# Performance work log

Measured on AMD Instinct MI355X. Metric: run time of the kernel, lower is better.

## Reference

```python
import jax, jax.numpy as jnp
import numpy as np

B, T, C, E, K = 4, 4096, 2048, 64, 8


def setup_inputs() -> dict:
    key = jax.random.key(0)
    k1, k2, k3 = jax.random.split(key, 3)
    hidden_states = jax.random.normal(k1, (B, T, C), dtype=jnp.float32)
    mask = jax.random.randint(k2, (B, T), 0, 2).astype(bool)
    gate_weight = jax.random.normal(k3, (E, C), dtype=jnp.float32) * 0.02
    gate_bias = jnp.zeros((E,), dtype=jnp.float32)
    expert_biases = jnp.zeros((E,), dtype=jnp.float32)
    return {
        "hidden_states": hidden_states,
        "mask": mask,
        "gate_weight": gate_weight,
        "gate_bias": gate_bias,
        "expert_biases": expert_biases,
    }


def reference(hidden_states, mask, gate_weight, gate_bias, expert_biases):
    Bc, Tc, Cc = hidden_states.shape
    n_experts = gate_weight.shape[0]
    x = hidden_states.reshape(-1, Cc)                 # [N, C]
    m = mask.reshape(-1)                              # [N]
    gate_output = x @ gate_weight.T + gate_bias       # [N, E]
    gate_probs = jax.nn.sigmoid(gate_output)
    gate_logits = gate_output + expert_biases
    _, top_k_indices = jax.lax.top_k(gate_logits, K)  # [N, K]
    top_k_probs = jnp.take_along_axis(gate_probs, top_k_indices, axis=-1)
    top_k_probs = top_k_probs / jnp.sum(top_k_probs, axis=-1, keepdims=True)
    # masked bincount of routed experts (only tokens where mask is True)
    weights = jnp.broadcast_to(m[:, None], top_k_indices.shape).astype(jnp.float32)
    expert_counts = jnp.zeros((n_experts,), jnp.float32).at[top_k_indices.reshape(-1)].add(weights.reshape(-1))
    avg_count = expert_counts.mean()
    maxvio = (expert_counts.max() - avg_count) / (avg_count + 1e-5)
    # note: the in-place expert_biases sign-update is a training-time, no-grad
    # side effect and does not change the returned values of this call.
    return top_k_indices, top_k_probs, maxvio
```

## Files before the change

### kernel.cpp

```cpp
#include <hip/hip_runtime.h>
#include <math.h>

#define NTOK   16384
#define CDIM   2048
#define NEXP   64
#define TOPK   8
#define GBLK   1024
#define NWAVE  8

typedef _Float16 f16x8 __attribute__((ext_vector_type(8)));
typedef float    f32x4 __attribute__((ext_vector_type(4)));

__global__ __launch_bounds__(256) void pack_w16_kernel(
    const float* __restrict__ W,
    _Float16* __restrict__ Wh, _Float16* __restrict__ Wl)
{
    int t    = blockIdx.x * 256 + threadIdx.x;
    int lane = t & 63;
    int nt   = (t >> 6) & 3;
    int s    = t >> 8;
    int e    = nt * 16 + (lane & 15);
    int k    = s * 32 + (lane >> 4) * 8;
    const float* src = W + (size_t)e * CDIM + k;
    #pragma unroll
    for (int j = 0; j < 8; j++) {
        float x = src[j];
        _Float16 h = (_Float16)x;
        Wh[(size_t)t * 8 + j] = h;
        Wl[(size_t)t * 8 + j] = (_Float16)(x - (float)h);
    }
}

__device__ __forceinline__ void mfma_step(
    const float4 v0, const float4 v1,
    const f16x8* __restrict__ bh, const f16x8* __restrict__ bl,
    f32x4* __restrict__ acc)
{
    float xr[8] = {v0.x, v0.y, v0.z, v0.w, v1.x, v1.y, v1.z, v1.w};
    f16x8 ah, al;
    #pragma unroll
    for (int j = 0; j < 8; j++) {
        _Float16 h = (_Float16)xr[j];
        ah[j] = h;
        al[j] = (_Float16)(xr[j] - (float)h);
    }
    #pragma unroll
    for (int nt = 0; nt < 4; nt++) {
        acc[nt] = __builtin_amdgcn_mfma_f32_16x16x32_f16(ah, bh[nt], acc[nt], 0, 0, 0);
        acc[nt] = __builtin_amdgcn_mfma_f32_16x16x32_f16(al, bh[nt], acc[nt], 0, 0, 0);
        acc[nt] = __builtin_amdgcn_mfma_f32_16x16x32_f16(ah, bl[nt], acc[nt], 0, 0, 0);
    }
}

__global__ __launch_bounds__(512, 8) void gate_fused_kernel(
    const float* __restrict__ x,
    const _Float16* __restrict__ Wh,
    const _Float16* __restrict__ Wl,
    const int*   __restrict__ mask,
    const float* __restrict__ gbias,
    const float* __restrict__ ebias,
    float*       __restrict__ out,
    float*       __restrict__ blockcnt)
{
    __shared__ f32x4 sacc[NWAVE][4][64];
    __shared__ unsigned int cnt[NEXP];
    const int tid  = threadIdx.x;
    const int lane = tid & 63;
    const int wid  = tid >> 6;
    if (tid < NEXP) cnt[tid] = 0u;

    const int tok0 = blockIdx.x * 16;
    const int col  = lane & 15;
    const int q    = lane >> 4;
    const float* xp = x + (size_t)(tok0 + col) * CDIM + wid * 256 + q * 8;
    const f16x8* bhp = (const f16x8*)Wh + (size_t)wid * 8 * 256 + lane;
    const f16x8* blp = (const f16x8*)Wl + (size_t)wid * 8 * 256 + lane;

    f32x4 acc[4];
    #pragma unroll
    for (int nt = 0; nt < 4; nt++) acc[nt] = (f32x4){0.f, 0.f, 0.f, 0.f};

    #pragma unroll 2
    for (int s = 0; s < 8; s++) {
        float4 v0 = *(const float4*)(xp + s * 32);
        float4 v1 = *(const float4*)(xp + s * 32 + 4);
        f16x8 bh[4], bl[4];
        #pragma unroll
        for (int nt = 0; nt < 4; nt++) {
            bh[nt] = bhp[s * 256 + nt * 64];
            bl[nt] = blp[s * 256 + nt * 64];
        }
        mfma_step(v0, v1, bh, bl, acc);
    }

    #pragma unroll
    for (int nt = 0; nt < 4; nt++) sacc[wid][nt][lane] = acc[nt];
    __syncthreads();

    if (wid == 0) {
        f32x4 zv[4];
        #pragma unroll
        for (int nt = 0; nt < 4; nt++) {
            f32x4 s = sacc[0][nt][lane];
            #pragma unroll
            for (int w = 1; w < NWAVE; w++) s += sacc[w][nt][lane];
            zv[nt] = s;
        }

        float gb[4], eb[4];
        #pragma unroll
        for (int nt = 0; nt < 4; nt++) {
            gb[nt] = gbias[nt * 16 + col];
            eb[nt] = ebias[nt * 16 + col];
        }

        #pragma unroll
        for (int r = 0; r < 4; r++) {
            const int t = tok0 + q * 4 + r;
            float z[4], sel[4];
            #pragma unroll
            for (int nt = 0; nt < 4; nt++) {
                z[nt]   = zv[nt][r] + gb[nt];
                sel[nt] = z[nt] + eb[nt];
            }

            int idxs[TOPK]; float probs[TOPK]; float psum = 0.f;
            #pragma unroll
            for (int rr = 0; rr < TOPK; rr++) {
                float bv = -INFINITY, bz = 0.f; int bidx = 1 << 30;
                #pragma unroll
                for (int nt = 0; nt < 4; nt++)
                    if (sel[nt] > bv) { bv = sel[nt]; bz = z[nt]; bidx = nt * 16 + col; }
                #pragma unroll
                for (int m = 1; m < 16; m <<= 1) {
                    float ov = __shfl_xor(bv, m);
                    float oz = __shfl_xor(bz, m);
                    int   oi = __shfl_xor(bidx, m);
                    if (ov > bv || (ov == bv && oi < bidx)) { bv = ov; bz = oz; bidx = oi; }
                }
                idxs[rr] = bidx;
                float p = 1.f / (1.f + expf(-bz));
                probs[rr] = p; psum += p;
                if ((bidx & 15) == col) sel[bidx >> 4] = -INFINITY;
            }
            float inv = 1.f / psum;
            if (col < TOPK) {
                out[(size_t)t * TOPK + col] = (float)idxs[col];
                out[(size_t)NTOK * TOPK + (size_t)t * TOPK + col] = probs[col] * inv;
                if (mask[t] != 0) atomicAdd(&cnt[idxs[col]], 1u);
            }
        }
        blockcnt[(size_t)blockIdx.x * NEXP + lane] = (float)cnt[lane];
    }
}

__global__ __launch_bounds__(256) void finalize_kernel(
    const float* __restrict__ blockcnt, float* __restrict__ out)
{
    __shared__ float ps[4][NEXP];
    const int t = threadIdx.x;
    const int e = t & 63, c = t >> 6;
    float s = 0.f;
    #pragma unroll 8
    for (int b = 0; b < GBLK / 4; b++)
        s += blockcnt[(size_t)(c * (GBLK / 4) + b) * NEXP + e];
    ps[c][e] = s;
    __syncthreads();
    if (t < 64) {
        float tot = ps[0][t] + ps[1][t] + ps[2][t] + ps[3][t];
        float mx = tot, sm = tot;
        #pragma unroll
        for (int o = 32; o > 0; o >>= 1) {
            mx = fmaxf(mx, __shfl_down(mx, o));
            sm += __shfl_down(sm, o);
        }
        if (t == 0) {
            float avg = sm / (float)NEXP;
            out[2 * NTOK * TOPK] = (mx - avg) / (avg + 1e-5f);
        }
    }
}

__global__ __launch_bounds__(256) void fused_fallback_kernel(
    const float* __restrict__ x, const int* __restrict__ mask,
    const float* __restrict__ W, const float* __restrict__ gbias,
    const float* __restrict__ ebias, float* __restrict__ out,
    unsigned int* __restrict__ counts)
{
    __shared__ float As[64][36];
    __shared__ float Bs[64][36];
    __shared__ float Lg[64][NEXP + 1];
    __shared__ float s_gb[NEXP], s_eb[NEXP];
    __shared__ unsigned int s_cnt[NEXP];
    const int tid = threadIdx.x;
    const int tx = tid & 15, ty = tid >> 4;
    const int m0 = blockIdx.x * 64;
    if (tid < NEXP) { s_gb[tid] = gbias[tid]; s_eb[tid] = ebias[tid]; s_cnt[tid] = 0u; }
    float acc[4][4] = {};
    for (int kb = 0; kb < CDIM; kb += 32) {
        __syncthreads();
        #pragma unroll
        for (int p = 0; p < 2; p++) {
            int lin = tid + p * 256; int m = lin >> 3; int c4 = (lin & 7) << 2;
            *(float4*)&As[m][c4] = *(const float4*)&x[(size_t)(m0 + m) * CDIM + kb + c4];
            *(float4*)&Bs[m][c4] = *(const float4*)&W[(size_t)m * CDIM + kb + c4];
        }
        __syncthreads();
        #pragma unroll
        for (int k4 = 0; k4 < 32; k4 += 4) {
            float4 a[4], b[4];
            #pragma unroll
            for (int i = 0; i < 4; i++) a[i] = *(const float4*)&As[ty * 4 + i][k4];
            #pragma unroll
            for (int j = 0; j < 4; j++) b[j] = *(const float4*)&Bs[tx * 4 + j][k4];
            #pragma unroll
            for (int i = 0; i < 4; i++)
                #pragma unroll
                for (int j = 0; j < 4; j++)
                    acc[i][j] += a[i].x * b[j].x + a[i].y * b[j].y
                               + a[i].z * b[j].z + a[i].w * b[j].w;
        }
    }
    __syncthreads();
    #pragma unroll
    for (int i = 0; i < 4; i++)
        #pragma unroll
        for (int j = 0; j < 4; j++)
            Lg[ty * 4 + i][tx * 4 + j] = acc[i][j] + s_gb[tx * 4 + j];
    __syncthreads();
    if (tid < 64) {
        const int g = m0 + tid;
        unsigned long long used = 0ull;
        int idxs[TOPK]; float probs[TOPK]; float psum = 0.f;
        #pragma unroll
        for (int k = 0; k < TOPK; k++) {
            float best = -INFINITY; int bi = 0;
            for (int n = 0; n < NEXP; n++) {
                if ((used >> n) & 1ull) continue;
                float vv = Lg[tid][n] + s_eb[n];
                if (vv > best) { best = vv; bi = n; }
            }
            used |= (1ull << bi);
            idxs[k] = bi;
            float p = 1.f / (1.f + expf(-Lg[tid][bi]));
            probs[k] = p; psum += p;
        }
        float inv = 1.f / psum;
        #pragma unroll
        for (int k = 0; k < TOPK; k++) {
            out[(size_t)g * TOPK + k] = (float)idxs[k];
            out[(size_t)NTOK * TOPK + (size_t)g * TOPK + k] = probs[k] * inv;
        }
        if (mask[g] != 0)
            #pragma unroll
            for (int k = 0; k < TOPK; k++) atomicAdd(&s_cnt[idxs[k]], 1u);
    }
    __syncthreads();
    if (tid < NEXP && s_cnt[tid] != 0u) atomicAdd(&counts[tid], s_cnt[tid]);
}

__global__ void finalize_atomic_kernel(const unsigned int* __restrict__ counts,
                                       float* __restrict__ out)
{
    const int t = threadIdx.x;
    float c  = (float)counts[t];
    float mx = c, sm = c;
    #pragma unroll
    for (int o = 32; o > 0; o >>= 1) {
        mx = fmaxf(mx, __shfl_down(mx, o));
        sm += __shfl_down(sm, o);
    }
    if (t == 0) {
        float avg = sm / (float)NEXP;
        out[2 * NTOK * TOPK] = (mx - avg) / (avg + 1e-5f);
    }
}

extern "C" void kernel_launch(void* const* d_in, const int* in_sizes, int n_in,
                              void* d_out, int out_size, void* d_ws, size_t ws_size,
                              hipStream_t stream)
{
    const float* x     = (const float*)d_in[0];
    const int*   mask  = (const int*)  d_in[1];
    const float* W     = (const float*)d_in[2];
    const float* gbias = (const float*)d_in[3];
    const float* ebias = (const float*)d_in[4];
    float* out = (float*)d_out;

    const size_t whB  = (size_t)NEXP * CDIM * sizeof(_Float16);
    const size_t bcB  = (size_t)GBLK * NEXP * sizeof(float);
    const size_t need = 2 * whB + bcB;

    if (ws_size >= need) {
        _Float16* Wh = (_Float16*)d_ws;
        _Float16* Wl = (_Float16*)((char*)d_ws + whB);
        float* blockcnt = (float*)((char*)d_ws + 2 * whB);

        pack_w16_kernel<<<64, 256, 0, stream>>>(W, Wh, Wl);
        gate_fused_kernel<<<GBLK, 512, 0, stream>>>(x, Wh, Wl, mask, gbias, ebias, out, blockcnt);
        finalize_kernel<<<1, 256, 0, stream>>>(blockcnt, out);
        return;
    }

    unsigned int* counts = (unsigned int*)d_ws;
    hipMemsetAsync(d_ws, 0, NEXP * sizeof(unsigned int), stream);
    fused_fallback_kernel<<<NTOK / 64, 256, 0, stream>>>(x, mask, W, gbias, ebias, out, counts);
    finalize_atomic_kernel<<<1, 64, 0, stream>>>(counts, out);
}
```

Before: 270.0 us.

## Process 32 tokens per block to reuse gate weight fragments across two tiles

Each block now computes two 16-token tiles, so every loaded split-f16 weight fragment feeds both tiles' MFMA chains. This halves the grid size and the weight reads per token. Top-k selection for the two tiles runs on two waves instead of one, and the per-block count write moves after an extra barrier. The cost is more registers (occupancy hint lowered from 8 to 4 waves) and a doubled shared accumulator buffer.

```diff
diff --git a/kernel.cpp b/kernel.cpp
--- a/kernel.cpp
+++ b/kernel.cpp
@@ -5,8 +5,9 @@
 #define CDIM   2048
 #define NEXP   64
 #define TOPK   8
-#define GBLK   1024
+#define TOKB   32
 #define NWAVE  8
+#define GBLK   (NTOK / TOKB)
 
 typedef _Float16 f16x8 __attribute__((ext_vector_type(8)));
 typedef float    f32x4 __attribute__((ext_vector_type(4)));
@@ -31,28 +32,19 @@
     }
 }
 
-__device__ __forceinline__ void mfma_step(
-    const float4 v0, const float4 v1,
-    const f16x8* __restrict__ bh, const f16x8* __restrict__ bl,
-    f32x4* __restrict__ acc)
+__device__ __forceinline__ void split_f16(
+    const float4 v0, const float4 v1, f16x8& ah, f16x8& al)
 {
     float xr[8] = {v0.x, v0.y, v0.z, v0.w, v1.x, v1.y, v1.z, v1.w};
-    f16x8 ah, al;
     #pragma unroll
     for (int j = 0; j < 8; j++) {
         _Float16 h = (_Float16)xr[j];
         ah[j] = h;
         al[j] = (_Float16)(xr[j] - (float)h);
     }
-    #pragma unroll
-    for (int nt = 0; nt < 4; nt++) {
-        acc[nt] = __builtin_amdgcn_mfma_f32_16x16x32_f16(ah, bh[nt], acc[nt], 0, 0, 0);
-        acc[nt] = __builtin_amdgcn_mfma_f32_16x16x32_f16(al, bh[nt], acc[nt], 0, 0, 0);
-        acc[nt] = __builtin_amdgcn_mfma_f32_16x16x32_f16(ah, bl[nt], acc[nt], 0, 0, 0);
-    }
-}
-
-__global__ __launch_bounds__(512, 8) void gate_fused_kernel(
+}
+
+__global__ __launch_bounds__(512, 4) void gate_fused_kernel(
     const float* __restrict__ x,
     const _Float16* __restrict__ Wh,
     const _Float16* __restrict__ Wl,
@@ -62,48 +54,69 @@
     float*       __restrict__ out,
     float*       __restrict__ blockcnt)
 {
-    __shared__ f32x4 sacc[NWAVE][4][64];
+    __shared__ f32x4 sacc[NWAVE][2][4][64];
     __shared__ unsigned int cnt[NEXP];
     const int tid  = threadIdx.x;
     const int lane = tid & 63;
     const int wid  = tid >> 6;
     if (tid < NEXP) cnt[tid] = 0u;
 
-    const int tok0 = blockIdx.x * 16;
+    const int tok0 = blockIdx.x * TOKB;
     const int col  = lane & 15;
     const int q    = lane >> 4;
-    const float* xp = x + (size_t)(tok0 + col) * CDIM + wid * 256 + q * 8;
+    const float* xpA = x + (size_t)(tok0 + col) * CDIM + wid * 256 + q * 8;
+    const float* xpB = xpA + (size_t)16 * CDIM;
     const f16x8* bhp = (const f16x8*)Wh + (size_t)wid * 8 * 256 + lane;
     const f16x8* blp = (const f16x8*)Wl + (size_t)wid * 8 * 256 + lane;
 
-    f32x4 acc[4];
-    #pragma unroll
-    for (int nt = 0; nt < 4; nt++) acc[nt] = (f32x4){0.f, 0.f, 0.f, 0.f};
+    f32x4 accA[4], accB[4];
+    #pragma unroll
+    for (int nt = 0; nt < 4; nt++) {
+        accA[nt] = (f32x4){0.f, 0.f, 0.f, 0.f};
+        accB[nt] = (f32x4){0.f, 0.f, 0.f, 0.f};
+    }
 
     #pragma unroll 2
     for (int s = 0; s < 8; s++) {
-        float4 v0 = *(const float4*)(xp + s * 32);
-        float4 v1 = *(const float4*)(xp + s * 32 + 4);
+        float4 a0 = *(const float4*)(xpA + s * 32);
+        float4 a1 = *(const float4*)(xpA + s * 32 + 4);
+        float4 c0 = *(const float4*)(xpB + s * 32);
+        float4 c1 = *(const float4*)(xpB + s * 32 + 4);
         f16x8 bh[4], bl[4];
         #pragma unroll
         for (int nt = 0; nt < 4; nt++) {
             bh[nt] = bhp[s * 256 + nt * 64];
             bl[nt] = blp[s * 256 + nt * 64];
         }
-        mfma_step(v0, v1, bh, bl, acc);
-    }
-
-    #pragma unroll
-    for (int nt = 0; nt < 4; nt++) sacc[wid][nt][lane] = acc[nt];
-    __syncthreads();
-
-    if (wid == 0) {
+        f16x8 ahA, alA, ahB, alB;
+        split_f16(a0, a1, ahA, alA);
+        split_f16(c0, c1, ahB, alB);
+        #pragma unroll
+        for (int nt = 0; nt < 4; nt++) {
+            accA[nt] = __builtin_amdgcn_mfma_f32_16x16x32_f16(ahA, bh[nt], accA[nt], 0, 0, 0);
+            accA[nt] = __builtin_amdgcn_mfma_f32_16x16x32_f16(alA, bh[nt], accA[nt], 0, 0, 0);
+            accA[nt] = __builtin_amdgcn_mfma_f32_16x16x32_f16(ahA, bl[nt], accA[nt], 0, 0, 0);
+            accB[nt] = __builtin_amdgcn_mfma_f32_16x16x32_f16(ahB, bh[nt], accB[nt], 0, 0, 0);
+            accB[nt] = __builtin_amdgcn_mfma_f32_16x16x32_f16(alB, bh[nt], accB[nt], 0, 0, 0);
+            accB[nt] = __builtin_amdgcn_mfma_f32_16x16x32_f16(ahB, bl[nt], accB[nt], 0, 0, 0);
+        }
+    }
+
+    #pragma unroll
+    for (int nt = 0; nt < 4; nt++) {
+        sacc[wid][0][nt][lane] = accA[nt];
+        sacc[wid][1][nt][lane] = accB[nt];
+    }
+    __syncthreads();
+
+    if (wid < 2) {
+        const int ts = wid;
         f32x4 zv[4];
         #pragma unroll
         for (int nt = 0; nt < 4; nt++) {
-            f32x4 s = sacc[0][nt][lane];
-            #pragma unroll
-            for (int w = 1; w < NWAVE; w++) s += sacc[w][nt][lane];
+            f32x4 s = sacc[0][ts][nt][lane];
+            #pragma unroll
+            for (int w = 1; w < NWAVE; w++) s += sacc[w][ts][nt][lane];
             zv[nt] = s;
         }
 
@@ -116,7 +129,7 @@
 
         #pragma unroll
         for (int r = 0; r < 4; r++) {
-            const int t = tok0 + q * 4 + r;
+            const int t = tok0 + ts * 16 + q * 4 + r;
             float z[4], sel[4];
             #pragma unroll
             for (int nt = 0; nt < 4; nt++) {
@@ -150,8 +163,10 @@
                 if (mask[t] != 0) atomicAdd(&cnt[idxs[col]], 1u);
             }
         }
-        blockcnt[(size_t)blockIdx.x * NEXP + lane] = (float)cnt[lane];
-    }
+    }
+    __syncthreads();
+    if (tid < NEXP)
+        blockcnt[(size_t)blockIdx.x * NEXP + tid] = (float)cnt[tid];
 }
 
 __global__ __launch_bounds__(256) void finalize_kernel(
```

Measured after the change: 229.1 us. -15.2%, faster.
